# Optimization experiments

Hardware: AMD Instinct MI355X
Metric: run time of the kernel (lower is better)

## Reference

```python
import jax, jax.numpy as jnp
import numpy as np


def setup_inputs() -> dict:
    key = jax.random.key(0)
    ks = jax.random.split(key, 7)
    B, Q, K, H, D, R = 2, 2048, 2048, 16, 64, 32
    queries = jax.random.normal(ks[0], (B, Q, H, D), dtype=jnp.float32)
    keys = jax.random.normal(ks[1], (B, K, H, D), dtype=jnp.float32)
    values = jax.random.normal(ks[2], (B, K, H, D), dtype=jnp.float32)
    att_mask = jax.random.randint(ks[3], (B, Q, K), 0, 2, dtype=jnp.int32)
    relative_att_ids = jax.random.randint(ks[4], (B, Q, K), 0, R, dtype=jnp.int32)
    # TruncatedNormal(stddev=0.5) approximated by clipped normal
    relative_emb_table = jnp.clip(
        0.5 * jax.random.normal(ks[5], (R, H, D), dtype=jnp.float32), -1.0, 1.0)
    relative_bias_table = jnp.zeros((R, H), dtype=jnp.float32)
    return {
        'queries': queries,
        'keys': keys,
        'values': values,
        'att_mask': att_mask,
        'relative_att_ids': relative_att_ids,
        'relative_emb_table': relative_emb_table,
        'relative_bias_table': relative_bias_table,
    }


def reference(queries, keys, values, att_mask, relative_att_ids,
              relative_emb_table, relative_bias_table):
    # content scores: [B,Q,K,H]
    content = jnp.einsum('bqhd,bkhd->bqkh', queries, keys)
    # relative scores per vocab id: [B,Q,R,H]
    all_rel = jnp.einsum('bqhd,rhd->bqrh', queries, relative_emb_table)
    all_rel = all_rel + relative_bias_table  # broadcast [R,H]
    # gather along vocab axis per (q,k): [B,Q,K,H]
    rel = jnp.take_along_axis(
        all_rel, relative_att_ids[:, :, :, None].astype(jnp.int32), axis=2)
    scores = content + rel
    d = queries.shape[-1]
    scores = scores / jnp.sqrt(jnp.asarray(d, scores.dtype))
    mask_adder = -10000.0 * (1.0 - att_mask[:, :, :, None].astype(scores.dtype))
    scores = scores + mask_adder
    probs = jax.nn.softmax(scores, axis=-2)  # softmax over key axis
    return jnp.einsum('bqkh,bkhd->bqhd', probs, values)
```

## Files before the change

### kernel.cpp

```cpp
#include <hip/hip_runtime.h>
#include <hip/hip_fp16.h>
#include <stdint.h>

#define Bn 2
#define Qn 2048
#define Kn 2048
#define Hn 16
#define Dn 64
#define Rn 32

#define LOG2E_8 0.18033688011112042f
#define MASK_NEG -14426.950408889634f

typedef __attribute__((ext_vector_type(8))) short short8v;
typedef __attribute__((ext_vector_type(4))) float f32x4;
typedef __attribute__((ext_vector_type(4))) uint32_t u32x4;

static __device__ __forceinline__ uint16_t bf16rn(float f) {
  uint32_t u = __builtin_bit_cast(uint32_t, f);
  u += 0x7FFFu + ((u >> 16) & 1u);
  return (uint16_t)(u >> 16);
}
static __device__ __forceinline__ float exp2a(float x) {
  float r; asm("v_exp_f32 %0, %1" : "=v"(r) : "v"(x)); return r;
}
static __device__ __forceinline__ uint32_t cvtpk(float lo, float hi) {
  uint32_t r; asm("v_cvt_pk_bf16_f32 %0, %1, %2" : "=v"(r) : "v"(lo), "v"(hi)); return r;
}
static __device__ __forceinline__ void gl_lds16(const void* g, void* l) {
  __builtin_amdgcn_global_load_lds((const __attribute__((address_space(1))) void*)g,
                                   (__attribute__((address_space(3))) void*)l, 16, 0, 0);
}

__global__ void pack_kernel(const int* __restrict__ ids,
                            const int* __restrict__ msk,
                            uint32_t* __restrict__ outp, int n4) {
  int i = blockIdx.x * 256 + threadIdx.x;
  if (i >= n4) return;
  int4 a = reinterpret_cast<const int4*>(ids)[i];
  int4 m = reinterpret_cast<const int4*>(msk)[i];
  uint32_t v = (uint32_t)((a.x | (m.x << 5)) & 0x3f)
             | ((uint32_t)((a.y | (m.y << 5)) & 0x3f) << 8)
             | ((uint32_t)((a.z | (m.z << 5)) & 0x3f) << 16)
             | ((uint32_t)((a.w | (m.w << 5)) & 0x3f) << 24);
  outp[i] = v;
}

__global__ __launch_bounds__(256) void kfrag6_kernel(const float* __restrict__ Kg,
                                                     const float* __restrict__ Vg,
                                                     uint8_t* __restrict__ frag) {
  const int bid = blockIdx.x;
  const int c = bid & 63;
  const int h = (bid >> 6) & 15;
  const int b = bid >> 10;
  uint8_t* panel = frag + (size_t)(b * 16 + h) * 524288u + (size_t)c * 8192u;
  uint4* kf = reinterpret_cast<uint4*>(panel);
  uint4* vf = reinterpret_cast<uint4*>(panel + 4096);
  const int tid = threadIdx.x;
  const int sdq = tid & 7, srow = (tid >> 3) & 15, stile = tid >> 7;
  const int sg = sdq & 3, sdm = sdq >> 2;
  const float* kp = Kg + ((((size_t)b * Kn) + c * 32 + stile * 16 + srow) * Hn + h) * Dn + (sdm * 32 + sg * 4);
  const float4 x0 = *reinterpret_cast<const float4*>(kp);
  const float4 x1 = *reinterpret_cast<const float4*>(kp + 16);
  const float xs0[4] = {x0.x * LOG2E_8, x0.y * LOG2E_8, x0.z * LOG2E_8, x0.w * LOG2E_8};
  const float xs1[4] = {x1.x * LOG2E_8, x1.y * LOG2E_8, x1.z * LOG2E_8, x1.w * LOG2E_8};
  uint4 uh;
  uh.x = bf16rn(xs0[0]) | ((uint32_t)bf16rn(xs0[1]) << 16);
  uh.y = bf16rn(xs0[2]) | ((uint32_t)bf16rn(xs0[3]) << 16);
  uh.z = bf16rn(xs1[0]) | ((uint32_t)bf16rn(xs1[1]) << 16);
  uh.w = bf16rn(xs1[2]) | ((uint32_t)bf16rn(xs1[3]) << 16);
  kf[(stile * 2 + sdm) * 64 + (srow + 16 * sg)] = uh;
  const int vd = tid & 63, vkq = tid >> 6;
  const float* vp = Vg + ((((size_t)b * Kn) + c * 32 + vkq * 4) * Hn + h) * Dn + vd;
  float v0[4], v1[4];
#pragma unroll
  for (int i = 0; i < 4; ++i) {
    v0[i] = vp[i * (Hn * Dn)];
    v1[i] = vp[(16 + i) * (Hn * Dn)];
  }
  uint4 uv;
  uv.x = bf16rn(v0[0]) | ((uint32_t)bf16rn(v0[1]) << 16);
  uv.y = bf16rn(v0[2]) | ((uint32_t)bf16rn(v0[3]) << 16);
  uv.z = bf16rn(v1[0]) | ((uint32_t)bf16rn(v1[1]) << 16);
  uv.w = bf16rn(v1[2]) | ((uint32_t)bf16rn(v1[3]) << 16);
  vf[(vd >> 4) * 64 + (vd & 15) + 16 * vkq] = uv;
}

__global__ __launch_bounds__(256) void tab_kernel(const float* __restrict__ Qg,
                                                  const float* __restrict__ Eg,
                                                  const float* __restrict__ biasg,
                                                  __half* __restrict__ tabg) {
  __shared__ alignas(16) char smem[25856];
  float* const q_lds = reinterpret_cast<float*>(smem);
  float* const et    = reinterpret_cast<float*>(smem + 17408);
  const int tid = threadIdx.x;
  const int bid = blockIdx.x;
  const int qt = bid & 31;
  const int h  = (bid >> 5) & 15;
  const int b  = bid >> 9;
  const int q0 = qt * 64;
  {
    const int row = tid >> 2, dq = (tid & 3) * 16;
    const float4* s4 = reinterpret_cast<const float4*>(
        Qg + (((size_t)b * Qn + q0 + row) * Hn + h) * Dn + dq);
    float4* dst = reinterpret_cast<float4*>(&q_lds[row * 68 + dq]);
#pragma unroll
    for (int i = 0; i < 4; ++i) dst[i] = s4[i];
  }
  {
    const int r = tid >> 3, d0 = (tid & 7) * 8;
    const float* src = Eg + ((r * Hn + h) * Dn + d0);
#pragma unroll
    for (int i = 0; i < 8; ++i) et[(d0 + i) * 33 + r] = src[i];
  }
  __syncthreads();
  {
    const int r = tid & 31, q8 = tid >> 5;
    float a8[8] = {0.f, 0.f, 0.f, 0.f, 0.f, 0.f, 0.f, 0.f};
    const float bias = biasg[r * Hn + h];
    for (int d = 0; d < 64; ++d) {
      const float e = et[d * 33 + r];
#pragma unroll
      for (int i = 0; i < 8; ++i) a8[i] += e * q_lds[(q8 * 8 + i) * 68 + d];
    }
#pragma unroll
    for (int i = 0; i < 8; ++i) {
      const float ar = LOG2E_8 * (a8[i] + bias);
      const size_t rowo = ((size_t)(b * 16 + h) * 2048 + q0 + q8 * 8 + i) * 64;
      tabg[rowo + r]      = __float2half(ar + MASK_NEG);
      tabg[rowo + 32 + r] = __float2half(ar);
    }
  }
}

__global__ __launch_bounds__(512, 4) void attn8_kernel(
    const float* __restrict__ Qg, const uint8_t* __restrict__ packed,
    const uint8_t* __restrict__ kfragp, const __half* __restrict__ tabg,
    float* __restrict__ outg) {
  __shared__ alignas(16) char smem[49152];
  const int tid = threadIdx.x;
  const int lane = tid & 63;
  const int w = tid >> 6;
  const int w4 = w & 3;
  const int ks = w >> 2;
  const int qr = lane & 15;
  const int g = lane >> 4;

  const int wi = (blockIdx.x & 7) * 64 + (blockIdx.x >> 3);
  const int qt = wi & 15;
  const int h = (wi >> 4) & 15;
  const int b = wi >> 8;
  const int q0 = qt * 128;

  char* const myhalf = smem + 16384 + ks * 16384;

  {
    const uint8_t* tsrc = reinterpret_cast<const uint8_t*>(
        tabg + ((size_t)(b * 16 + h) * 2048 + q0) * 64);
    char* ld = smem + w * 2048;
    gl_lds16(tsrc + (size_t)w * 2048 + (size_t)lane * 16, ld);
    gl_lds16(tsrc + (size_t)w * 2048 + 1024 + (size_t)lane * 16, ld + 1024);
  }
  const uint8_t* sbase = kfragp + (size_t)(b * 16 + h) * 524288u +
                         (size_t)(ks * 32) * 8192u + (size_t)w4 * 2048 + (size_t)lane * 16;
  {
    char* ld = myhalf + w4 * 2048;
    gl_lds16(sbase, ld);
    gl_lds16(sbase + 1024, ld + 1024);
  }

  short8v qhi[2][2];
#pragma unroll
  for (int t = 0; t < 2; ++t)
#pragma unroll
    for (int dm = 0; dm < 2; ++dm) {
      const float* qp = Qg + (((size_t)b * Qn + q0 + w4 * 32 + t * 16 + qr) * Hn + h) * Dn +
                        dm * 32 + 4 * g;
      const float4 x0 = *reinterpret_cast<const float4*>(qp);
      const float4 x1 = *reinterpret_cast<const float4*>(qp + 16);
      u32x4 u;
      u[0] = cvtpk(x0.x, x0.y); u[1] = cvtpk(x0.z, x0.w);
      u[2] = cvtpk(x1.x, x1.y); u[3] = cvtpk(x1.z, x1.w);
      qhi[t][dm] = __builtin_bit_cast(short8v, u);
    }

  int64_t prow[2];
  int trow[2];
#pragma unroll
  for (int t = 0; t < 2; ++t) {
    prow[t] = ((int64_t)(b * Qn + q0 + w4 * 32 + t * 16 + qr)) * Kn + ks * 1024 + 4 * g;
    trow[t] = (w4 * 32 + t * 16 + qr) * 64;
  }
  uint32_t pc[2][2], pn[2][2] = {{0u, 0u}, {0u, 0u}};
#pragma unroll
  for (int t = 0; t < 2; ++t)
#pragma unroll
    for (int st = 0; st < 2; ++st)
      pc[t][st] = *reinterpret_cast<const uint32_t*>(packed + prow[t] + st * 16);

  asm volatile("s_waitcnt vmcnt(0)" ::: "memory");
  __builtin_amdgcn_sched_barrier(0);
  __syncthreads();

  const short8v ones = {(short)0x3F80, (short)0x3F80, (short)0x3F80, (short)0x3F80,
                        (short)0x3F80, (short)0x3F80, (short)0x3F80, (short)0x3F80};
  const __half* tabh = reinterpret_cast<const __half*>(smem);

  f32x4 acc[2][4] = {{{0.f,0.f,0.f,0.f},{0.f,0.f,0.f,0.f},{0.f,0.f,0.f,0.f},{0.f,0.f,0.f,0.f}},
                     {{0.f,0.f,0.f,0.f},{0.f,0.f,0.f,0.f},{0.f,0.f,0.f,0.f},{0.f,0.f,0.f,0.f}}};
  f32x4 accl[2] = {{0.f,0.f,0.f,0.f},{0.f,0.f,0.f,0.f}};
  int cbuf = 0;

  for (int c = 0; c < 32; ++c) {
    if (c + 1 < 32) {
      const uint8_t* gs = sbase + (size_t)(c + 1) * 8192u;
      char* ld = myhalf + (cbuf ^ 1) * 8192 + w4 * 2048;
      gl_lds16(gs, ld);
      gl_lds16(gs + 1024, ld + 1024);
      const int64_t kb = (int64_t)(c + 1) * 32;
#pragma unroll
      for (int t = 0; t < 2; ++t)
#pragma unroll
        for (int st = 0; st < 2; ++st)
          pn[t][st] = *reinterpret_cast<const uint32_t*>(packed + prow[t] + kb + st * 16);
    }

    const short8v* kfs = reinterpret_cast<const short8v*>(myhalf + cbuf * 8192);
    f32x4 s[2][2] = {{{0.f,0.f,0.f,0.f},{0.f,0.f,0.f,0.f}},
                     {{0.f,0.f,0.f,0.f},{0.f,0.f,0.f,0.f}}};
    __builtin_amdgcn_s_setprio(1);
#pragma unroll
    for (int dm = 0; dm < 2; ++dm) {
      const short8v k0 = kfs[dm * 64 + lane];
      const short8v k1 = kfs[(2 + dm) * 64 + lane];
#pragma unroll
      for (int t = 0; t < 2; ++t) {
        s[t][0] = __builtin_amdgcn_mfma_f32_16x16x32_bf16(k0, qhi[t][dm], s[t][0], 0, 0, 0);
        s[t][1] = __builtin_amdgcn_mfma_f32_16x16x32_bf16(k1, qhi[t][dm], s[t][1], 0, 0, 0);
      }
    }
    __builtin_amdgcn_s_setprio(0);

    const short8v* vfs = reinterpret_cast<const short8v*>(myhalf + cbuf * 8192 + 4096);
    short8v vv[4];
#pragma unroll
    for (int dt = 0; dt < 4; ++dt) vv[dt] = vfs[dt * 64 + lane];

#pragma unroll
    for (int t = 0; t < 2; ++t) {
      float pv[8];
#pragma unroll
      for (int i = 0; i < 8; ++i) {
        const int st = i >> 2, r = i & 3;
        const uint32_t v = (pc[t][st] >> (8 * r)) & 63u;
        pv[i] = exp2a(s[t][st][r] + __half2float(tabh[trow[t] + (int)v]));
      }
      u32x4 pu;
      pu[0] = cvtpk(pv[0], pv[1]); pu[1] = cvtpk(pv[2], pv[3]);
      pu[2] = cvtpk(pv[4], pv[5]); pu[3] = cvtpk(pv[6], pv[7]);
      const short8v pa = __builtin_bit_cast(short8v, pu);
      __builtin_amdgcn_s_setprio(1);
#pragma unroll
      for (int dt = 0; dt < 4; ++dt)
        acc[t][dt] = __builtin_amdgcn_mfma_f32_16x16x32_bf16(pa, vv[dt], acc[t][dt], 0, 0, 0);
      accl[t] = __builtin_amdgcn_mfma_f32_16x16x32_bf16(pa, ones, accl[t], 0, 0, 0);
      __builtin_amdgcn_s_setprio(0);
    }

#pragma unroll
    for (int t = 0; t < 2; ++t) { pc[t][0] = pn[t][0]; pc[t][1] = pn[t][1]; }

    asm volatile("s_waitcnt vmcnt(0)" ::: "memory");
    __builtin_amdgcn_sched_barrier(0);
    __syncthreads();
    cbuf ^= 1;
  }

  float* const acc1s = reinterpret_cast<float*>(smem + 16384);
  float* const l1s   = reinterpret_cast<float*>(smem);
  if (ks == 1) {
#pragma unroll
    for (int t = 0; t < 2; ++t) {
#pragma unroll
      for (int dt = 0; dt < 4; ++dt)
#pragma unroll
        for (int r = 0; r < 4; ++r)
          acc1s[(w4 * 32 + t * 16 + 4 * g + r) * 64 + dt * 16 + qr] = acc[t][dt][r];
#pragma unroll
      for (int r = 0; r < 4; ++r)
        l1s[w4 * 32 + t * 16 + 4 * g + r] = accl[t][r];
    }
  }
  __syncthreads();
  if (ks == 0) {
#pragma unroll
    for (int t = 0; t < 2; ++t) {
      const f32x4 l1v = *reinterpret_cast<const f32x4*>(&l1s[w4 * 32 + t * 16 + 4 * g]);
      f32x4 linv;
#pragma unroll
      for (int r = 0; r < 4; ++r) linv[r] = 1.0f / (accl[t][r] + l1v[r]);
#pragma unroll
      for (int dt = 0; dt < 4; ++dt)
#pragma unroll
        for (int r = 0; r < 4; ++r) {
          const int lrow = w4 * 32 + t * 16 + 4 * g + r;
          const float o = (acc[t][dt][r] + acc1s[lrow * 64 + dt * 16 + qr]) * linv[r];
          outg[(((size_t)b * Qn + q0 + lrow) * Hn + h) * Dn + dt * 16 + qr] = o;
        }
    }
  }
}

__global__ __launch_bounds__(256) void attn_old_kernel(
    const float* __restrict__ Qg, const float* __restrict__ Kg,
    const float* __restrict__ Vg, const int* __restrict__ maskg,
    const int* __restrict__ idsg, const float* __restrict__ Eg,
    const float* __restrict__ biasg, float* __restrict__ outg) {
  __shared__ alignas(16) char smem[34304];
  float* const allrel = reinterpret_cast<float*>(smem);
  float* const q_lds  = reinterpret_cast<float*>(smem + 8448);
  float* const et_lds = reinterpret_cast<float*>(smem + 25856);
  uint4* const kfrag  = reinterpret_cast<uint4*>(smem + 8448);
  uint4* const vfrag  = reinterpret_cast<uint4*>(smem + 16640);

  const int tid  = threadIdx.x;
  const int lane = tid & 63;
  const int w    = tid >> 6;
  const int qr   = lane & 15;
  const int g    = lane >> 4;

  const int bid = blockIdx.x;
  const int h  = bid & 15;
  const int qt = (bid >> 4) & 31;
  const int b  = bid >> 9;
  const int q0 = qt * 64;

  {
    const int row = tid >> 2, dq = (tid & 3) * 16;
    const float4* s4 =
        reinterpret_cast<const float4*>(Qg + (((b * Qn) + q0 + row) * Hn + h) * Dn + dq);
    float4* dst = reinterpret_cast<float4*>(&q_lds[row * 68 + dq]);
#pragma unroll
    for (int i = 0; i < 4; ++i) dst[i] = s4[i];
  }
  {
    const int r = tid >> 3, d0 = (tid & 7) * 8;
    const float* src = Eg + ((r * Hn + h) * Dn + d0);
#pragma unroll
    for (int i = 0; i < 8; ++i) et_lds[(d0 + i) * 33 + r] = src[i];
  }
  __syncthreads();

  const int qloc = w * 16 + qr;
  short8v qhi[2], qlo[2];
#pragma unroll
  for (int dm = 0; dm < 2; ++dm) {
#pragma unroll
    for (int j = 0; j < 8; ++j) {
      const int dl = (j < 4) ? (4 * g + j) : (16 + 4 * g + (j - 4));
      const float x = q_lds[qloc * 68 + dm * 32 + dl];
      const uint16_t hi = bf16rn(x);
      qhi[dm][j] = (short)hi;
      const float lo = x - __builtin_bit_cast(float, (uint32_t)hi << 16);
      qlo[dm][j] = (short)bf16rn(lo);
    }
  }

  {
    const int r = tid & 31, q8 = tid >> 5;
    float acc[8] = {0.f, 0.f, 0.f, 0.f, 0.f, 0.f, 0.f, 0.f};
    const float bias = biasg[r * Hn + h];
    for (int d = 0; d < 64; ++d) {
      const float e = et_lds[d * 33 + r];
#pragma unroll
      for (int i = 0; i < 8; ++i) acc[i] += e * q_lds[(q8 * 8 + i) * 68 + d];
    }
#pragma unroll
    for (int i = 0; i < 8; ++i)
      allrel[(q8 * 8 + i) * 33 + r] = 0.125f * (acc[i] + bias);
  }
  __syncthreads();

  const int sdq = tid & 7, srow = (tid >> 3) & 15, stile = tid >> 7;
  const int sg = sdq & 3, sdm = sdq >> 2;
  int koff = (((b * Kn) + stile * 16 + srow) * Hn + h) * Dn + (sdm * 32 + sg * 4);
  const int kslotH = (stile * 2 + sdm) * 64 + (srow + 16 * sg);
  const int kslotL = (4 + stile * 2 + sdm) * 64 + (srow + 16 * sg);
  const int vd = tid & 63, vkq = tid >> 6;
  int voff = (((b * Kn) + vkq * 4) * Hn + h) * Dn + vd;
  const int vslot = (vd >> 4) * 64 + (vd & 15) + 16 * vkq;

  const int qglob = q0 + qloc;
  const int prow = (b * Qn + qglob) * Kn + 4 * g;

  f32x4 acc[4] = {{0.f,0.f,0.f,0.f},{0.f,0.f,0.f,0.f},{0.f,0.f,0.f,0.f},{0.f,0.f,0.f,0.f}};
  float mrun = -1e30f, lrun = 0.f;

  const short8v* kfs = reinterpret_cast<const short8v*>(kfrag);
  const short8v* vfs = reinterpret_cast<const short8v*>(vfrag);

  for (int c = 0; c < 64; ++c) {
    const int kb = c * 32;
    __syncthreads();
    {
      const float4 x0 = *reinterpret_cast<const float4*>(Kg + koff);
      const float4 x1 = *reinterpret_cast<const float4*>(Kg + koff + 16);
      koff += 32 * Hn * Dn;
      const float xs0[4] = {x0.x, x0.y, x0.z, x0.w};
      const float xs1[4] = {x1.x, x1.y, x1.z, x1.w};
      uint16_t hh[8], ll[8];
#pragma unroll
      for (int i = 0; i < 4; ++i) {
        const uint16_t h0 = bf16rn(xs0[i]);
        const uint16_t h1 = bf16rn(xs1[i]);
        hh[i] = h0; hh[4 + i] = h1;
        ll[i] = bf16rn(xs0[i] - __builtin_bit_cast(float, (uint32_t)h0 << 16));
        ll[4 + i] = bf16rn(xs1[i] - __builtin_bit_cast(float, (uint32_t)h1 << 16));
      }
      uint4 uh, ul;
      uh.x = hh[0] | ((uint32_t)hh[1] << 16); uh.y = hh[2] | ((uint32_t)hh[3] << 16);
      uh.z = hh[4] | ((uint32_t)hh[5] << 16); uh.w = hh[6] | ((uint32_t)hh[7] << 16);
      ul.x = ll[0] | ((uint32_t)ll[1] << 16); ul.y = ll[2] | ((uint32_t)ll[3] << 16);
      ul.z = ll[4] | ((uint32_t)ll[5] << 16); ul.w = ll[6] | ((uint32_t)ll[7] << 16);
      kfrag[kslotH] = uh;
      kfrag[kslotL] = ul;
    }
    {
      float v0[4], v1[4];
#pragma unroll
      for (int i = 0; i < 4; ++i) {
        v0[i] = Vg[voff + i * (Hn * Dn)];
        v1[i] = Vg[voff + 16 * Hn * Dn + i * (Hn * Dn)];
      }
      voff += 32 * Hn * Dn;
      uint4 uv;
      uv.x = bf16rn(v0[0]) | ((uint32_t)bf16rn(v0[1]) << 16);
      uv.y = bf16rn(v0[2]) | ((uint32_t)bf16rn(v0[3]) << 16);
      uv.z = bf16rn(v1[0]) | ((uint32_t)bf16rn(v1[1]) << 16);
      uv.w = bf16rn(v1[2]) | ((uint32_t)bf16rn(v1[3]) << 16);
      vfrag[vslot] = uv;
    }
    __syncthreads();

    f32x4 s0 = {0.f, 0.f, 0.f, 0.f}, s1 = {0.f, 0.f, 0.f, 0.f};
#pragma unroll
    for (int dm = 0; dm < 2; ++dm) {
      const short8v k0h = kfs[(dm) * 64 + lane];
      const short8v k1h = kfs[(2 + dm) * 64 + lane];
      const short8v k0l = kfs[(4 + dm) * 64 + lane];
      const short8v k1l = kfs[(6 + dm) * 64 + lane];
      s0 = __builtin_amdgcn_mfma_f32_16x16x32_bf16(k0h, qhi[dm], s0, 0, 0, 0);
      s1 = __builtin_amdgcn_mfma_f32_16x16x32_bf16(k1h, qhi[dm], s1, 0, 0, 0);
      s0 = __builtin_amdgcn_mfma_f32_16x16x32_bf16(k0h, qlo[dm], s0, 0, 0, 0);
      s1 = __builtin_amdgcn_mfma_f32_16x16x32_bf16(k1h, qlo[dm], s1, 0, 0, 0);
      s0 = __builtin_amdgcn_mfma_f32_16x16x32_bf16(k0l, qhi[dm], s0, 0, 0, 0);
      s1 = __builtin_amdgcn_mfma_f32_16x16x32_bf16(k1l, qhi[dm], s1, 0, 0, 0);
    }

    float sv[8];
    {
      const int ib = prow + kb;
      const int4 i0 = *reinterpret_cast<const int4*>(idsg + ib);
      const int4 i1 = *reinterpret_cast<const int4*>(idsg + ib + 16);
      const int4 m0 = *reinterpret_cast<const int4*>(maskg + ib);
      const int4 m1 = *reinterpret_cast<const int4*>(maskg + ib + 16);
      const int ia0[4] = {i0.x, i0.y, i0.z, i0.w};
      const int ia1[4] = {i1.x, i1.y, i1.z, i1.w};
      const int ma0[4] = {m0.x, m0.y, m0.z, m0.w};
      const int ma1[4] = {m1.x, m1.y, m1.z, m1.w};
#pragma unroll
      for (int r = 0; r < 4; ++r) {
        sv[r]     = 0.125f * s0[r] + allrel[qloc * 33 + ia0[r]] + (ma0[r] ? 0.f : -10000.f);
        sv[4 + r] = 0.125f * s1[r] + allrel[qloc * 33 + ia1[r]] + (ma1[r] ? 0.f : -10000.f);
      }
    }

    float m8 = sv[0];
#pragma unroll
    for (int i = 1; i < 8; ++i) m8 = fmaxf(m8, sv[i]);
    m8 = fmaxf(m8, __shfl_xor(m8, 16));
    m8 = fmaxf(m8, __shfl_xor(m8, 32));
    const float mnew = fmaxf(mrun, m8);
    const float sc = __expf(mrun - mnew);
    mrun = mnew;
    float pv[8];
    float ps = 0.f;
#pragma unroll
    for (int i = 0; i < 8; ++i) { pv[i] = __expf(sv[i] - mnew); ps += pv[i]; }
    ps += __shfl_xor(ps, 16);
    ps += __shfl_xor(ps, 32);
    lrun = lrun * sc + ps;

    f32x4 scv;
#pragma unroll
    for (int r = 0; r < 4; ++r) scv[r] = __shfl(sc, 4 * g + r);
#pragma unroll
    for (int dt = 0; dt < 4; ++dt) acc[dt] *= scv;

    short8v pa;
#pragma unroll
    for (int i = 0; i < 8; ++i) pa[i] = (short)bf16rn(pv[i]);
#pragma unroll
    for (int dt = 0; dt < 4; ++dt)
      acc[dt] = __builtin_amdgcn_mfma_f32_16x16x32_bf16(pa, vfs[dt * 64 + lane], acc[dt], 0, 0, 0);
  }

  const float linv = 1.0f / lrun;
  f32x4 lv;
#pragma unroll
  for (int r = 0; r < 4; ++r) lv[r] = __shfl(linv, 4 * g + r);
#pragma unroll
  for (int dt = 0; dt < 4; ++dt) {
#pragma unroll
    for (int r = 0; r < 4; ++r) {
      const int qrow = q0 + w * 16 + 4 * g + r;
      outg[(((b * Qn) + qrow) * Hn + h) * Dn + dt * 16 + qr] = acc[dt][r] * lv[r];
    }
  }
}

extern "C" void kernel_launch(void* const* d_in, const int* in_sizes, int n_in,
                              void* d_out, int out_size, void* d_ws, size_t ws_size,
                              hipStream_t stream) {
  const float* Qg    = (const float*)d_in[0];
  const float* Kg    = (const float*)d_in[1];
  const float* Vg    = (const float*)d_in[2];
  const int*   maskg = (const int*)d_in[3];
  const int*   idsg  = (const int*)d_in[4];
  const float* Eg    = (const float*)d_in[5];
  const float* biasg = (const float*)d_in[6];
  float* outg = (float*)d_out;

  const size_t oPack = 0;
  const size_t oK    = 8388608;
  const size_t oT    = 25165824;
  const size_t need8 = 33554432;
  const int n4 = (Bn * Qn * Kn) / 4;

  uint8_t* ws = (uint8_t*)d_ws;

  if (ws_size >= need8) {
    pack_kernel<<<n4 / 256, 256, 0, stream>>>(idsg, maskg, (uint32_t*)(ws + oPack), n4);
    kfrag6_kernel<<<Bn * Hn * 64, 256, 0, stream>>>(Kg, Vg, ws + oK);
    tab_kernel<<<Bn * Hn * 32, 256, 0, stream>>>(Qg, Eg, biasg, (__half*)(ws + oT));
    attn8_kernel<<<Bn * Hn * (Qn / 128), 512, 0, stream>>>(
        Qg, ws + oPack, ws + oK, (const __half*)(ws + oT), outg);
  } else {
    attn_old_kernel<<<Bn * Hn * (Qn / 64), 256, 0, stream>>>(
        Qg, Kg, Vg, maskg, idsg, Eg, biasg, outg);
  }
}
```

Before: 114.3 us.

## Triple-buffer K/V LDS prefetch and compute relative table with MFMA

Makes the attention kernel's K/V fragment staging triple-buffered, with loads issued two chunks ahead and a partial vmcnt wait, so global-to-LDS latency overlaps more compute. The relative-score table kernel switches from scalar FMA loops over LDS to bf16 MFMA with hi/lo splitting to keep it close to fp32. LDS per block grows from 48 KB to 64 KB, which may limit occupancy at the requested 4 blocks per CU. The vmcnt(6) count must match the number of outstanding loads exactly or results become racy.

New measurement: 111.9 us. -2.1%, faster.

```diff
diff --git a/kernel.cpp b/kernel.cpp
--- a/kernel.cpp
+++ b/kernel.cpp
@@ -20,6 +20,9 @@
   uint32_t u = __builtin_bit_cast(uint32_t, f);
   u += 0x7FFFu + ((u >> 16) & 1u);
   return (uint16_t)(u >> 16);
+}
+static __device__ __forceinline__ float bf16f(uint16_t h) {
+  return __builtin_bit_cast(float, (uint32_t)h << 16);
 }
 static __device__ __forceinline__ float exp2a(float x) {
   float r; asm("v_exp_f32 %0, %1" : "=v"(r) : "v"(x)); return r;
@@ -86,58 +89,81 @@
   vf[(vd >> 4) * 64 + (vd & 15) + 16 * vkq] = uv;
 }
 
-__global__ __launch_bounds__(256) void tab_kernel(const float* __restrict__ Qg,
-                                                  const float* __restrict__ Eg,
-                                                  const float* __restrict__ biasg,
-                                                  __half* __restrict__ tabg) {
-  __shared__ alignas(16) char smem[25856];
-  float* const q_lds = reinterpret_cast<float*>(smem);
-  float* const et    = reinterpret_cast<float*>(smem + 17408);
+__global__ __launch_bounds__(256) void tab2_kernel(const float* __restrict__ Qg,
+                                                   const float* __restrict__ Eg,
+                                                   const float* __restrict__ biasg,
+                                                   __half* __restrict__ tabg) {
   const int tid = threadIdx.x;
+  const int lane = tid & 63;
+  const int w = tid >> 6;
+  const int qr = lane & 15;
+  const int g = lane >> 4;
   const int bid = blockIdx.x;
   const int qt = bid & 31;
-  const int h  = (bid >> 5) & 15;
-  const int b  = bid >> 9;
-  const int q0 = qt * 64;
-  {
-    const int row = tid >> 2, dq = (tid & 3) * 16;
-    const float4* s4 = reinterpret_cast<const float4*>(
-        Qg + (((size_t)b * Qn + q0 + row) * Hn + h) * Dn + dq);
-    float4* dst = reinterpret_cast<float4*>(&q_lds[row * 68 + dq]);
-#pragma unroll
-    for (int i = 0; i < 4; ++i) dst[i] = s4[i];
-  }
-  {
-    const int r = tid >> 3, d0 = (tid & 7) * 8;
-    const float* src = Eg + ((r * Hn + h) * Dn + d0);
-#pragma unroll
-    for (int i = 0; i < 8; ++i) et[(d0 + i) * 33 + r] = src[i];
-  }
-  __syncthreads();
-  {
-    const int r = tid & 31, q8 = tid >> 5;
-    float a8[8] = {0.f, 0.f, 0.f, 0.f, 0.f, 0.f, 0.f, 0.f};
-    const float bias = biasg[r * Hn + h];
-    for (int d = 0; d < 64; ++d) {
-      const float e = et[d * 33 + r];
-#pragma unroll
-      for (int i = 0; i < 8; ++i) a8[i] += e * q_lds[(q8 * 8 + i) * 68 + d];
-    }
-#pragma unroll
-    for (int i = 0; i < 8; ++i) {
-      const float ar = LOG2E_8 * (a8[i] + bias);
-      const size_t rowo = ((size_t)(b * 16 + h) * 2048 + q0 + q8 * 8 + i) * 64;
-      tabg[rowo + r]      = __float2half(ar + MASK_NEG);
-      tabg[rowo + 32 + r] = __float2half(ar);
-    }
-  }
-}
-
-__global__ __launch_bounds__(512, 4) void attn8_kernel(
+  const int h = (bid >> 5) & 15;
+  const int b = bid >> 9;
+  const int q0 = qt * 64 + w * 16;
+
+  short8v eh[2][2], el[2][2];
+#pragma unroll
+  for (int rt = 0; rt < 2; ++rt)
+#pragma unroll
+    for (int dm = 0; dm < 2; ++dm) {
+      const float* ep = Eg + (((size_t)(rt * 16 + qr) * Hn + h) * Dn) + dm * 32 + 4 * g;
+      const float4 x0 = *reinterpret_cast<const float4*>(ep);
+      const float4 x1 = *reinterpret_cast<const float4*>(ep + 16);
+      const float xs[8] = {x0.x * LOG2E_8, x0.y * LOG2E_8, x0.z * LOG2E_8, x0.w * LOG2E_8,
+                           x1.x * LOG2E_8, x1.y * LOG2E_8, x1.z * LOG2E_8, x1.w * LOG2E_8};
+#pragma unroll
+      for (int j = 0; j < 8; ++j) {
+        const uint16_t hi = bf16rn(xs[j]);
+        eh[rt][dm][j] = (short)hi;
+        el[rt][dm][j] = (short)bf16rn(xs[j] - bf16f(hi));
+      }
+    }
+  short8v qh[2], ql[2];
+#pragma unroll
+  for (int dm = 0; dm < 2; ++dm) {
+    const float* qp = Qg + (((size_t)b * Qn + q0 + qr) * Hn + h) * Dn + dm * 32 + 4 * g;
+    const float4 x0 = *reinterpret_cast<const float4*>(qp);
+    const float4 x1 = *reinterpret_cast<const float4*>(qp + 16);
+    const float xs[8] = {x0.x, x0.y, x0.z, x0.w, x1.x, x1.y, x1.z, x1.w};
+#pragma unroll
+    for (int j = 0; j < 8; ++j) {
+      const uint16_t hi = bf16rn(xs[j]);
+      qh[dm][j] = (short)hi;
+      ql[dm][j] = (short)bf16rn(xs[j] - bf16f(hi));
+    }
+  }
+#pragma unroll
+  for (int rt = 0; rt < 2; ++rt) {
+    f32x4 d;
+#pragma unroll
+    for (int j = 0; j < 4; ++j)
+      d[j] = LOG2E_8 * biasg[(rt * 16 + 4 * g + j) * Hn + h];
+#pragma unroll
+    for (int dm = 0; dm < 2; ++dm) {
+      d = __builtin_amdgcn_mfma_f32_16x16x32_bf16(eh[rt][dm], qh[dm], d, 0, 0, 0);
+      d = __builtin_amdgcn_mfma_f32_16x16x32_bf16(el[rt][dm], qh[dm], d, 0, 0, 0);
+      d = __builtin_amdgcn_mfma_f32_16x16x32_bf16(eh[rt][dm], ql[dm], d, 0, 0, 0);
+    }
+    const size_t rowo = ((size_t)(b * 16 + h) * 2048 + q0 + qr) * 64;
+    union { ushort4 u4; __half hh[4]; } um, uu;
+#pragma unroll
+    for (int j = 0; j < 4; ++j) {
+      um.hh[j] = __float2half(d[j] + MASK_NEG);
+      uu.hh[j] = __float2half(d[j]);
+    }
+    *reinterpret_cast<ushort4*>(&tabg[rowo + rt * 16 + 4 * g]) = um.u4;
+    *reinterpret_cast<ushort4*>(&tabg[rowo + 32 + rt * 16 + 4 * g]) = uu.u4;
+  }
+}
+
+__global__ __launch_bounds__(512, 4) void attn9_kernel(
     const float* __restrict__ Qg, const uint8_t* __restrict__ packed,
     const uint8_t* __restrict__ kfragp, const __half* __restrict__ tabg,
     float* __restrict__ outg) {
-  __shared__ alignas(16) char smem[49152];
+  __shared__ alignas(16) char smem[65536];
   const int tid = threadIdx.x;
   const int lane = tid & 63;
   const int w = tid >> 6;
@@ -152,7 +178,24 @@
   const int b = wi >> 8;
   const int q0 = qt * 128;
 
-  char* const myhalf = smem + 16384 + ks * 16384;
+  char* const myhalf = smem + 16384 + ks * 24576;
+  char* bA = myhalf;
+  char* bB = myhalf + 8192;
+  char* bC = myhalf + 16384;
+
+  int64_t prow[2];
+  int trow[2];
+#pragma unroll
+  for (int t = 0; t < 2; ++t) {
+    prow[t] = ((int64_t)(b * Qn + q0 + w4 * 32 + t * 16 + qr)) * Kn + ks * 1024 + 4 * g;
+    trow[t] = (w4 * 32 + t * 16 + qr) * 64;
+  }
+  uint32_t pc[2][2], pn[2][2] = {{0u, 0u}, {0u, 0u}};
+#pragma unroll
+  for (int t = 0; t < 2; ++t)
+#pragma unroll
+    for (int st = 0; st < 2; ++st)
+      pc[t][st] = *reinterpret_cast<const uint32_t*>(packed + prow[t] + st * 16);
 
   {
     const uint8_t* tsrc = reinterpret_cast<const uint8_t*>(
@@ -164,9 +207,12 @@
   const uint8_t* sbase = kfragp + (size_t)(b * 16 + h) * 524288u +
                          (size_t)(ks * 32) * 8192u + (size_t)w4 * 2048 + (size_t)lane * 16;
   {
-    char* ld = myhalf + w4 * 2048;
-    gl_lds16(sbase, ld);
-    gl_lds16(sbase + 1024, ld + 1024);
+    char* ld0 = bA + w4 * 2048;
+    gl_lds16(sbase, ld0);
+    gl_lds16(sbase + 1024, ld0 + 1024);
+    char* ld1 = bB + w4 * 2048;
+    gl_lds16(sbase + 8192, ld1);
+    gl_lds16(sbase + 8192 + 1024, ld1 + 1024);
   }
 
   short8v qhi[2][2];
@@ -184,20 +230,6 @@
       qhi[t][dm] = __builtin_bit_cast(short8v, u);
     }
 
-  int64_t prow[2];
-  int trow[2];
-#pragma unroll
-  for (int t = 0; t < 2; ++t) {
-    prow[t] = ((int64_t)(b * Qn + q0 + w4 * 32 + t * 16 + qr)) * Kn + ks * 1024 + 4 * g;
-    trow[t] = (w4 * 32 + t * 16 + qr) * 64;
-  }
-  uint32_t pc[2][2], pn[2][2] = {{0u, 0u}, {0u, 0u}};
-#pragma unroll
-  for (int t = 0; t < 2; ++t)
-#pragma unroll
-    for (int st = 0; st < 2; ++st)
-      pc[t][st] = *reinterpret_cast<const uint32_t*>(packed + prow[t] + st * 16);
-
   asm volatile("s_waitcnt vmcnt(0)" ::: "memory");
   __builtin_amdgcn_sched_barrier(0);
   __syncthreads();
@@ -209,23 +241,24 @@
   f32x4 acc[2][4] = {{{0.f,0.f,0.f,0.f},{0.f,0.f,0.f,0.f},{0.f,0.f,0.f,0.f},{0.f,0.f,0.f,0.f}},
                      {{0.f,0.f,0.f,0.f},{0.f,0.f,0.f,0.f},{0.f,0.f,0.f,0.f},{0.f,0.f,0.f,0.f}}};
   f32x4 accl[2] = {{0.f,0.f,0.f,0.f},{0.f,0.f,0.f,0.f}};
-  int cbuf = 0;
 
   for (int c = 0; c < 32; ++c) {
     if (c + 1 < 32) {
-      const uint8_t* gs = sbase + (size_t)(c + 1) * 8192u;
-      char* ld = myhalf + (cbuf ^ 1) * 8192 + w4 * 2048;
+      const int64_t kb = (int64_t)(c + 1) * 32;
+#pragma unroll
+      for (int t = 0; t < 2; ++t)
+#pragma unroll
+        for (int st = 0; st < 2; ++st)
+          pn[t][st] = *reinterpret_cast<const uint32_t*>(packed + prow[t] + kb + st * 16);
+    }
+    if (c + 2 < 32) {
+      const uint8_t* gs = sbase + (size_t)(c + 2) * 8192u;
+      char* ld = bC + w4 * 2048;
       gl_lds16(gs, ld);
       gl_lds16(gs + 1024, ld + 1024);
-      const int64_t kb = (int64_t)(c + 1) * 32;
-#pragma unroll
-      for (int t = 0; t < 2; ++t)
-#pragma unroll
-        for (int st = 0; st < 2; ++st)
-          pn[t][st] = *reinterpret_cast<const uint32_t*>(packed + prow[t] + kb + st * 16);
-    }
-
-    const short8v* kfs = reinterpret_cast<const short8v*>(myhalf + cbuf * 8192);
+    }
+
+    const short8v* kfs = reinterpret_cast<const short8v*>(bA);
     f32x4 s[2][2] = {{{0.f,0.f,0.f,0.f},{0.f,0.f,0.f,0.f}},
                      {{0.f,0.f,0.f,0.f},{0.f,0.f,0.f,0.f}}};
     __builtin_amdgcn_s_setprio(1);
@@ -241,7 +274,7 @@
     }
     __builtin_amdgcn_s_setprio(0);
 
-    const short8v* vfs = reinterpret_cast<const short8v*>(myhalf + cbuf * 8192 + 4096);
+    const short8v* vfs = reinterpret_cast<const short8v*>(bA + 4096);
     short8v vv[4];
 #pragma unroll
     for (int dt = 0; dt < 4; ++dt) vv[dt] = vfs[dt * 64 + lane];
@@ -267,13 +300,19 @@
       __builtin_amdgcn_s_setprio(0);
     }
 
-#pragma unroll
-    for (int t = 0; t < 2; ++t) { pc[t][0] = pn[t][0]; pc[t][1] = pn[t][1]; }
-
-    asm volatile("s_waitcnt vmcnt(0)" ::: "memory");
+    if (c + 1 < 32) {
+#pragma unroll
+      for (int t = 0; t < 2; ++t) { pc[t][0] = pn[t][0]; pc[t][1] = pn[t][1]; }
+    }
+
+    if (c < 30) {
+      asm volatile("s_waitcnt vmcnt(6)" ::: "memory");
+    } else {
+      asm volatile("s_waitcnt vmcnt(0)" ::: "memory");
+    }
     __builtin_amdgcn_sched_barrier(0);
     __syncthreads();
-    cbuf ^= 1;
+    char* tmp = bA; bA = bB; bB = bC; bC = tmp;
   }
 
   float* const acc1s = reinterpret_cast<float*>(smem + 16384);
@@ -361,8 +400,7 @@
       const float x = q_lds[qloc * 68 + dm * 32 + dl];
       const uint16_t hi = bf16rn(x);
       qhi[dm][j] = (short)hi;
-      const float lo = x - __builtin_bit_cast(float, (uint32_t)hi << 16);
-      qlo[dm][j] = (short)bf16rn(lo);
+      qlo[dm][j] = (short)bf16rn(x - bf16f(hi));
     }
   }
 
@@ -414,8 +452,8 @@
         const uint16_t h0 = bf16rn(xs0[i]);
         const uint16_t h1 = bf16rn(xs1[i]);
         hh[i] = h0; hh[4 + i] = h1;
-        ll[i] = bf16rn(xs0[i] - __builtin_bit_cast(float, (uint32_t)h0 << 16));
-        ll[4 + i] = bf16rn(xs1[i] - __builtin_bit_cast(float, (uint32_t)h1 << 16));
+        ll[i] = bf16rn(xs0[i] - bf16f(h0));
+        ll[4 + i] = bf16rn(xs1[i] - bf16f(h1));
       }
       uint4 uh, ul;
       uh.x = hh[0] | ((uint32_t)hh[1] << 16); uh.y = hh[2] | ((uint32_t)hh[3] << 16);
@@ -534,16 +572,16 @@
   const size_t oPack = 0;
   const size_t oK    = 8388608;
   const size_t oT    = 25165824;
-  const size_t need8 = 33554432;
+  const size_t need9 = 33554432;
   const int n4 = (Bn * Qn * Kn) / 4;
 
   uint8_t* ws = (uint8_t*)d_ws;
 
-  if (ws_size >= need8) {
+  if (ws_size >= need9) {
     pack_kernel<<<n4 / 256, 256, 0, stream>>>(idsg, maskg, (uint32_t*)(ws + oPack), n4);
     kfrag6_kernel<<<Bn * Hn * 64, 256, 0, stream>>>(Kg, Vg, ws + oK);
-    tab_kernel<<<Bn * Hn * 32, 256, 0, stream>>>(Qg, Eg, biasg, (__half*)(ws + oT));
-    attn8_kernel<<<Bn * Hn * (Qn / 128), 512, 0, stream>>>(
+    tab2_kernel<<<Bn * Hn * 32, 256, 0, stream>>>(Qg, Eg, biasg, (__half*)(ws + oT));
+    attn9_kernel<<<Bn * Hn * (Qn / 128), 512, 0, stream>>>(
         Qg, ws + oPack, ws + oK, (const __half*)(ws + oT), outg);
   } else {
     attn_old_kernel<<<Bn * Hn * (Qn / 64), 256, 0, stream>>>(
```
